# Kernel optimization log

Hardware: AMD Instinct MI355X
Metric: run time of the kernel (lower is better)

The kernel has to match this reference:

```python
import jax, jax.numpy as jnp
import numpy as np

EMBED = 256
HEADS = 8
HEAD_DIM = EMBED // HEADS  # 32, even for RoPE
INIT_VAL = 1.0
HEADS_RANGE = 3.0


def rotate_every_two(x):
    # (x1, x2) -> (-x2, x1) on interleaved pairs of last dim
    x1 = x[..., ::2]
    x2 = x[..., 1::2]
    return jnp.stack([-x2, x1], axis=-1).reshape(x.shape)


def theta_shift(x, sin, cos):
    # x: [B, heads, H, W, D]; sin/cos: [H, W, D] broadcast over B, heads
    return x * cos + rotate_every_two(x) * sin


def rel_pos_2d(H, W):
    # RetNetRelPos2d: RoPE angles + per-head exponential decay mask
    angle = 1.0 / (10000.0 ** jnp.linspace(0.0, 1.0, HEAD_DIM // 2))
    angle = jnp.repeat(angle, 2)  # [D]
    idx = jnp.arange(H * W, dtype=jnp.float32)
    sin = jnp.sin(idx[:, None] * angle[None, :]).reshape(H, W, HEAD_DIM)
    cos = jnp.cos(idx[:, None] * angle[None, :]).reshape(H, W, HEAD_DIM)
    h_idx = jnp.arange(HEADS, dtype=jnp.float32)
    decay = jnp.log(1.0 - 2.0 ** (-INIT_VAL - HEADS_RANGE * h_idx / HEADS))  # [heads]
    gh, gw = jnp.meshgrid(jnp.arange(H), jnp.arange(W), indexing='ij')
    grid = jnp.stack([gh, gw], axis=-1).reshape(H * W, 2)  # [N,2]
    dist = jnp.abs(grid[:, None, :] - grid[None, :, :]).sum(-1)  # [N,N] L1 distance
    mask = dist[None, :, :].astype(jnp.float32) * decay[:, None, None]  # [heads,N,N]
    return sin, cos, mask


def setup_inputs() -> dict:
    key = jax.random.key(0)
    ks = jax.random.split(key, 8)
    B, H, W, C = 2, 48, 48, EMBED
    s = 0.02
    return {
        'x': jax.random.normal(ks[0], (B, H, W, C), jnp.float32),
        'Wq': jax.random.normal(ks[1], (C, C), jnp.float32) * s,
        'bq': jnp.zeros((C,), jnp.float32),
        'Wk': jax.random.normal(ks[2], (C, C), jnp.float32) * s,
        'bk': jnp.zeros((C,), jnp.float32),
        'Wv': jax.random.normal(ks[3], (C, C), jnp.float32) * s,
        'bv': jnp.zeros((C,), jnp.float32),
        'lepe_w': jax.random.normal(ks[4], (C, 1, 5, 5), jnp.float32) * s,  # depthwise 5x5
        'lepe_b': jnp.zeros((C,), jnp.float32),
        'Wo': jax.random.normal(ks[5], (C, C), jnp.float32) * s,
        'bo': jnp.zeros((C,), jnp.float32),
    }


def reference(x, Wq, bq, Wk, bk, Wv, bv, lepe_w, lepe_b, Wo, bo):
    B, H, W, C = x.shape
    N = H * W
    sin, cos, mask = rel_pos_2d(H, W)
    scaling = HEAD_DIM ** -0.5

    q = x @ Wq + bq
    k = (x @ Wk + bk) * scaling
    v = x @ Wv + bv

    # lepe: depthwise 5x5 conv on v (BHWC)
    lepe = jax.lax.conv_general_dilated(
        v.transpose(0, 3, 1, 2), lepe_w, (1, 1), 'SAME',
        feature_group_count=C, dimension_numbers=('NCHW', 'OIHW', 'NCHW'))
    lepe = lepe.transpose(0, 2, 3, 1) + lepe_b  # [B,H,W,C]

    def split_heads(t):
        return t.reshape(B, H, W, HEADS, HEAD_DIM).transpose(0, 3, 1, 2, 4)

    qr = theta_shift(split_heads(q), sin, cos).reshape(B, HEADS, N, HEAD_DIM)
    kr = theta_shift(split_heads(k), sin, cos).reshape(B, HEADS, N, HEAD_DIM)
    vv = split_heads(v).reshape(B, HEADS, N, HEAD_DIM)

    attn = jnp.einsum('bhnd,bhmd->bhnm', qr, kr) + mask[None]  # [B,heads,N,N]
    attn = jax.nn.softmax(attn, axis=-1)
    out = jnp.einsum('bhnm,bhmd->bhnd', attn, vv)
    out = out.transpose(0, 2, 1, 3).reshape(B, H, W, C)
    out = out + lepe
    return out @ Wo + bo
```

## Files before the change

kernel.cpp:

```cpp
#include <hip/hip_runtime.h>
#include <hip/hip_bf16.h>
#include <math.h>

#define NN 2304
#define ROWSZ 4608
#define SZ (ROWSZ*256)

typedef __attribute__((ext_vector_type(8))) short short8;
typedef __attribute__((ext_vector_type(4))) float f32x4;

__device__ __forceinline__ float bf2f(unsigned short u) {
    return __uint_as_float(((unsigned int)u) << 16);
}
__device__ __forceinline__ unsigned short f2bf(float f) {
    unsigned int u = __float_as_uint(f);
    u += 0x7FFFu + ((u >> 16) & 1u);
    return (unsigned short)(u >> 16);
}
__device__ __forceinline__ unsigned int pack_bf2(float a, float b) {
    return (unsigned int)f2bf(a) | ((unsigned int)f2bf(b) << 16);
}

__device__ __forceinline__ float ub2f(unsigned int v, int r) {
#if defined(__has_builtin)
#if __has_builtin(__builtin_amdgcn_cvt_f32_ubyte0)
    switch (r) {
        case 0: return __builtin_amdgcn_cvt_f32_ubyte0(v);
        case 1: return __builtin_amdgcn_cvt_f32_ubyte1(v);
        case 2: return __builtin_amdgcn_cvt_f32_ubyte2(v);
        default: return __builtin_amdgcn_cvt_f32_ubyte3(v);
    }
#else
    return (float)((v >> (8*r)) & 0xFFu);
#endif
#else
    return (float)((v >> (8*r)) & 0xFFu);
#endif
}

template<int F32>
__device__ __forceinline__ float ldin(const void* p, int i) {
    if constexpr (F32) return ((const float*)p)[i];
    else return bf2f(((const unsigned short*)p)[i]);
}

__global__ void detect_kernel(const unsigned int* __restrict__ x, int* __restrict__ flag) {
    int t = threadIdx.x;
    int cnt = 0;
    for (int i = t; i < 256; i += 64) {
        unsigned int e = (x[i] >> 7) & 0xFFu;
        cnt += (e < 87u || e > 167u) ? 1 : 0;
    }
    #pragma unroll
    for (int o = 32; o; o >>= 1) cnt += __shfl_down(cnt, o);
    if (t == 0) *flag = (cnt >= 32) ? 1 : 0;
}

__global__ __launch_bounds__(256) void dist_kernel(unsigned char* __restrict__ D,
                                                   float2* __restrict__ scT) {
    const int nq = blockIdx.x;
    const int yq = (nq*21846) >> 20, xq = nq - yq*48;
    unsigned int* drow = reinterpret_cast<unsigned int*>(D + (size_t)nq*NN);
    for (int idx = threadIdx.x; idx < 576; idx += 256) {
        const int kp0 = idx*4;
        unsigned int wv = 0;
        #pragma unroll
        for (int r = 0; r < 4; ++r) {
            int kp = kp0 + r;
            int yk = (kp*21846) >> 20;
            int xk = kp - yk*48;
            unsigned int dist = __usad((unsigned)yq, (unsigned)yk,
                                __usad((unsigned)xq, (unsigned)xk, 0u));
            wv |= dist << (8*r);
        }
        drow[idx] = wv;
    }
    if (threadIdx.x < 16) {
        const int j = threadIdx.x;
        const float ang = exp2f((float)j * (-0.8858474919699633f));
        float sv, cv;
        sincosf((float)nq * ang, &sv, &cv);
        scT[nq*16 + j] = make_float2(sv, cv);
    }
}

__global__ __launch_bounds__(256) void xprep_kernel(const void* __restrict__ x,
    const int* __restrict__ flag, unsigned short* __restrict__ xb)
{
    const int e = (blockIdx.x*256 + threadIdx.x) * 8;
    if (*flag) {
        const float* xp = (const float*)x + e;
        float4 a0 = *reinterpret_cast<const float4*>(xp);
        float4 a1 = *reinterpret_cast<const float4*>(xp + 4);
        uint4 o;
        o.x = pack_bf2(a0.x, a0.y); o.y = pack_bf2(a0.z, a0.w);
        o.z = pack_bf2(a1.x, a1.y); o.w = pack_bf2(a1.z, a1.w);
        *reinterpret_cast<uint4*>(xb + e) = o;
    } else {
        *reinterpret_cast<uint4*>(xb + e) =
            *reinterpret_cast<const uint4*>((const unsigned short*)x + e);
    }
}

__global__ __launch_bounds__(256) void wprep_kernel(
    const void* __restrict__ Wq, const void* __restrict__ bq,
    const void* __restrict__ Wk, const void* __restrict__ bk,
    const void* __restrict__ Wv, const void* __restrict__ bv,
    const void* __restrict__ Wo, const void* __restrict__ bo,
    const void* __restrict__ lw, const void* __restrict__ lb,
    const int* __restrict__ flag,
    unsigned short* __restrict__ Wt, float* __restrict__ bb,
    float* __restrict__ lwT)
{
    __shared__ float wsh[256][17];
    const int t = threadIdx.x;
    const int m = blockIdx.y;
    const int F = *flag;
    if (m == 4) {
        if (blockIdx.x != 0) return;
        float wv[25];
        #pragma unroll
        for (int j = 0; j < 25; ++j)
            wv[j] = F ? ((const float*)lw)[t*25 + j]
                      : bf2f(((const unsigned short*)lw)[t*25 + j]);
        #pragma unroll
        for (int j = 0; j < 25; ++j) lwT[j*256 + t] = wv[j];
        bb[4*256 + t] = F ? ((const float*)lb)[t]
                          : bf2f(((const unsigned short*)lb)[t]);
        return;
    }
    const int oc0 = blockIdx.x * 16;
    const void* W  = (m == 0) ? Wq : (m == 1) ? Wk : (m == 2) ? Wv : Wo;
    const void* bs = (m == 0) ? bq : (m == 1) ? bk : (m == 2) ? bv : bo;
    const float scale = (m == 1) ? 0.17677669529663687f * 1.4426950408889634f : 1.0f;
    #pragma unroll
    for (int j2 = 0; j2 < 16; ++j2)
        wsh[t][j2] = F ? ((const float*)W)[t*256 + oc0 + j2]
                       : bf2f(((const unsigned short*)W)[t*256 + oc0 + j2]);
    __syncthreads();
    const int j = t >> 4, seg = t & 15;
    unsigned int u[8];
    #pragma unroll
    for (int i = 0; i < 8; ++i) {
        float v0 = wsh[seg*16 + 2*i][j]     * scale;
        float v1 = wsh[seg*16 + 2*i + 1][j] * scale;
        u[i] = pack_bf2(v0, v1);
    }
    unsigned short* drow = Wt + ((size_t)(m*256 + oc0 + j))*256 + seg*16;
    *reinterpret_cast<uint4*>(drow)     = make_uint4(u[0], u[1], u[2], u[3]);
    *reinterpret_cast<uint4*>(drow + 8) = make_uint4(u[4], u[5], u[6], u[7]);
    if (blockIdx.x == 0)
        bb[m*256 + t] = (F ? ((const float*)bs)[t]
                           : bf2f(((const unsigned short*)bs)[t])) * scale;
}

__global__ __launch_bounds__(256) void qkv_mfma(
    const unsigned short* __restrict__ xb, const unsigned short* __restrict__ Wt,
    const float* __restrict__ bb, const float2* __restrict__ scT,
    unsigned short* __restrict__ q, unsigned short* __restrict__ k,
    unsigned short* __restrict__ v, unsigned short* __restrict__ vT)
{
    __shared__ __align__(16) char smem[43136];
    char* sc_lds = smem + 40960;
    const int t = threadIdx.x;
    const int w = t >> 6, lane = t & 63;
    const int q16 = lane & 15, quad = lane >> 4;
    const int m = blockIdx.y;
    const int tok0 = blockIdx.x * 16;
    const int b = (tok0 >= NN) ? 1 : 0;
    const int n0 = tok0 - b*NN;

    {
        float2 sv = scT[(size_t)(n0 + (t >> 4))*16 + (t & 15)];
        *reinterpret_cast<float2*>(sc_lds + (t >> 4)*136 + (t & 15)*8) = sv;
    }
    short8 af[8];
    #pragma unroll
    for (int kk = 0; kk < 8; ++kk)
        af[kk] = *reinterpret_cast<const short8*>(
            xb + (size_t)(tok0 + q16)*256 + kk*32 + quad*8);

    const unsigned short* Wm = Wt + (size_t)m*256*256;
    {
        const unsigned short* src = Wm + (size_t)t*256;
        #pragma unroll
        for (int s = 0; s < 4; ++s)
            *reinterpret_cast<uint4*>(smem + t*80 + s*16) =
                *reinterpret_cast<const uint4*>(src + s*8);
    }
    __syncthreads();

    f32x4 acc[4];
    #pragma unroll
    for (int tt = 0; tt < 4; ++tt) acc[tt] = (f32x4){0.f, 0.f, 0.f, 0.f};
    int cur = 0;
    for (int kk = 0; kk < 8; ++kk) {
        const int kkn = (kk < 7) ? kk + 1 : 7;
        uint4 nw[4];
        const unsigned short* src = Wm + (size_t)t*256 + kkn*32;
        #pragma unroll
        for (int s = 0; s < 4; ++s) nw[s] = *reinterpret_cast<const uint4*>(src + s*8);
        char* Wl = smem + cur*20480;
        #pragma unroll
        for (int tt = 0; tt < 4; ++tt) {
            short8 bf = *reinterpret_cast<const short8*>(
                Wl + (w*64 + tt*16 + q16)*80 + quad*16);
            acc[tt] = __builtin_amdgcn_mfma_f32_16x16x32_bf16(af[kk], bf, acc[tt], 0, 0, 0);
        }
        char* Wn = smem + (cur ^ 1)*20480;
        #pragma unroll
        for (int s = 0; s < 4; ++s)
            *reinterpret_cast<uint4*>(Wn + t*80 + s*16) = nw[s];
        __syncthreads();
        cur ^= 1;
    }

    char* ostage = smem;
    float bias[4];
    #pragma unroll
    for (int tt = 0; tt < 4; ++tt) bias[tt] = bb[m*256 + w*64 + tt*16 + q16];
    if (m < 2) {
        const int odd = q16 & 1;
        #pragma unroll
        for (int tt = 0; tt < 4; ++tt) {
            const int j = ((tt & 1) << 3) + (q16 >> 1);
            #pragma unroll
            for (int r = 0; r < 4; ++r) {
                const int tokL = quad*4 + r;
                float a = acc[tt][r] + bias[tt];
                float ap = __shfl_xor(a, 1);
                float2 sc = *reinterpret_cast<const float2*>(sc_lds + tokL*136 + j*8);
                float val = odd ? fmaf(a, sc.y, ap*sc.x) : fmaf(a, sc.y, -ap*sc.x);
                *reinterpret_cast<unsigned short*>(
                    ostage + tokL*528 + (w*64 + tt*16 + q16)*2) = f2bf(val);
            }
        }
    } else {
        #pragma unroll
        for (int tt = 0; tt < 4; ++tt) {
            #pragma unroll
            for (int r = 0; r < 4; ++r)
                *reinterpret_cast<unsigned short*>(
                    ostage + (quad*4 + r)*528 + (w*64 + tt*16 + q16)*2)
                    = f2bf(acc[tt][r] + bias[tt]);
        }
    }
    __syncthreads();
    unsigned short* dst = (m == 0) ? q : (m == 1) ? k : v;
    {
        char* p = ostage + (t >> 4)*528 + (t & 15)*32;
        uint4 a0 = *reinterpret_cast<uint4*>(p);
        uint4 a1 = *reinterpret_cast<uint4*>(p + 16);
        unsigned short* drow = dst + (size_t)(tok0 + (t >> 4))*256 + (t & 15)*16;
        *reinterpret_cast<uint4*>(drow)     = a0;
        *reinterpret_cast<uint4*>(drow + 8) = a1;
    }
    if (m == 2) {
        const int h = t >> 5, d = t & 31;
        unsigned int vp[8];
        #pragma unroll
        for (int i = 0; i < 8; ++i) {
            unsigned short e0 = *reinterpret_cast<unsigned short*>(
                ostage + (2*i)*528 + (h*32 + d)*2);
            unsigned short e1 = *reinterpret_cast<unsigned short*>(
                ostage + (2*i + 1)*528 + (h*32 + d)*2);
            vp[i] = (unsigned int)e0 | ((unsigned int)e1 << 16);
        }
        unsigned short* vt = vT + ((size_t)(b*8 + h)*32 + d)*NN + n0;
        *reinterpret_cast<uint4*>(vt)     = make_uint4(vp[0], vp[1], vp[2], vp[3]);
        *reinterpret_cast<uint4*>(vt + 8) = make_uint4(vp[4], vp[5], vp[6], vp[7]);
    }
}

__global__ __launch_bounds__(256) void lepe_kernel(const unsigned short* __restrict__ v,
    const float* __restrict__ lwT, const float* __restrict__ bb,
    unsigned short* __restrict__ lepe)
{
    int c = threadIdx.x;
    int pos = blockIdx.x;
    int b  = pos >= NN ? 1 : 0;
    int yx = pos - b*NN;
    int y  = (yx*21846) >> 20;
    int xx = yx - y*48;
    float acc = bb[4*256 + c];
    #pragma unroll
    for (int ky = 0; ky < 5; ++ky) {
        int yy = y + ky - 2;
        if ((unsigned)yy >= 48u) continue;
        #pragma unroll
        for (int kx = 0; kx < 5; ++kx) {
            int xc = xx + kx - 2;
            if ((unsigned)xc >= 48u) continue;
            acc = fmaf(bf2f(v[((b*NN + yy*48 + xc)<<8) + c]),
                       lwT[(ky*5 + kx)*256 + c], acc);
        }
    }
    lepe[(pos<<8) + c] = f2bf(acc);
}

template<int DIRECT>
__global__ __launch_bounds__(256) void attn_kernel(
    const unsigned short* __restrict__ q, const unsigned short* __restrict__ k,
    const unsigned short* __restrict__ vT, const unsigned char* __restrict__ D,
    unsigned short* __restrict__ o, float* __restrict__ pacc, float* __restrict__ pl)
{
    __shared__ char smem[27648];
    const int t = threadIdx.x;
    const int w = t >> 6, lane = t & 63;
    const int q16 = lane & 15, quad = lane >> 4;
    char* PsB = smem + 19456 + w*2048;
    const int bh = blockIdx.y, b = bh >> 3, h = bh & 7;
    const int q0 = blockIdx.x*64 + w*16;
    const int nq = q0 + q16;
    const float decay2 = log2f(1.0f - exp2f(-1.0f - 0.375f*(float)h));
    short8 qfrag = *reinterpret_cast<const short8*>(q + ((size_t)(b*NN + nq))*256 + h*32 + quad*8);
    f32x4 acc0 = {0.f,0.f,0.f,0.f}, acc1 = {0.f,0.f,0.f,0.f};
    const f32x4 zero = {0.f,0.f,0.f,0.f};
    float lacc = 0.0f;
    const unsigned short* kbase = k + (size_t)(b*NN)*256 + h*32;
    const unsigned short* vtb = vT + (size_t)bh*32*NN;
    const unsigned char* Dbase = D + (size_t)nq*NN + quad*4;
    const int skr = t >> 2, skp = t & 3;
    const int svd = t >> 3, svp = t & 7;
    const int psW = q16*16 + (quad & 1)*8;
    const int qsh = quad >> 1;
    const int nchunk = 36 / gridDim.z;
    const int kt0 = blockIdx.z * nchunk;

    {
        uint4 kraw = *reinterpret_cast<const uint4*>(kbase + (kt0*64 + skr)*256 + skp*8);
        uint4 vraw = *reinterpret_cast<const uint4*>(vtb + svd*NN + kt0*64 + svp*8);
        *reinterpret_cast<uint4*>(smem + skr*80 + skp*16) = kraw;
        *reinterpret_cast<uint4*>(smem + 5120 + svd*144 + svp*16) = vraw;
    }
    __syncthreads();

    int cur = 0;
    for (int kc = 0; kc < nchunk; ++kc) {
        const int kt = kt0 + kc;
        const int ktn = (kc + 1 < nchunk) ? kt + 1 : kt;
        uint4 nk = *reinterpret_cast<const uint4*>(kbase + (ktn*64 + skr)*256 + skp*8);
        uint4 nv = *reinterpret_cast<const uint4*>(vtb + svd*NN + ktn*64 + svp*8);
        unsigned int dw[4];
        #pragma unroll
        for (int tt = 0; tt < 4; ++tt)
            dw[tt] = *reinterpret_cast<const unsigned int*>(Dbase + kt*64 + tt*16);
        char* KsB = smem + cur*9728;
        char* VtB = KsB + 5120;
        f32x4 st[4];
        #pragma unroll
        for (int tt = 0; tt < 4; ++tt) {
            short8 kf = *reinterpret_cast<const short8*>(KsB + (tt*16 + q16)*80 + quad*16);
            st[tt] = __builtin_amdgcn_mfma_f32_16x16x32_bf16(kf, qfrag, zero, 0, 0, 0);
        }
        unsigned int pk[8];
        float lsum = 0.0f;
        #pragma unroll
        for (int tt = 0; tt < 4; ++tt) {
            float p[4];
            #pragma unroll
            for (int r = 0; r < 4; ++r) {
                p[r] = exp2f(fmaf(decay2, ub2f(dw[tt], r), st[tt][r]));
                lsum += p[r];
            }
            pk[tt*2]   = __builtin_amdgcn_perm(__float_as_uint(p[1]), __float_as_uint(p[0]), 0x07060302);
            pk[tt*2+1] = __builtin_amdgcn_perm(__float_as_uint(p[3]), __float_as_uint(p[2]), 0x07060302);
        }
        lacc += lsum;
        #pragma unroll
        for (int tt = 0; tt < 4; ++tt) {
            uint2 pp; pp.x = pk[tt*2]; pp.y = pk[tt*2+1];
            *reinterpret_cast<uint2*>(PsB + (tt >> 1)*1024 + (((tt*2) + qsh) & 3)*256 + psW) = pp;
        }
        #pragma unroll
        for (int kh = 0; kh < 2; ++kh) {
            short8 pf = *reinterpret_cast<const short8*>(PsB + kh*1024 + lane*16);
            short8 v0 = *reinterpret_cast<const short8*>(VtB + q16*144 + kh*64 + quad*16);
            short8 v1 = *reinterpret_cast<const short8*>(VtB + (16 + q16)*144 + kh*64 + quad*16);
            acc0 = __builtin_amdgcn_mfma_f32_16x16x32_bf16(v0, pf, acc0, 0, 0, 0);
            acc1 = __builtin_amdgcn_mfma_f32_16x16x32_bf16(v1, pf, acc1, 0, 0, 0);
        }
        char* KsN = smem + (cur^1)*9728;
        *reinterpret_cast<uint4*>(KsN + skr*80 + skp*16) = nk;
        *reinterpret_cast<uint4*>(KsN + 5120 + svd*144 + svp*16) = nv;
        __syncthreads();
        cur ^= 1;
    }
    lacc += __shfl_xor(lacc, 16);
    lacc += __shfl_xor(lacc, 32);
    if constexpr (DIRECT) {
        float invl = 1.0f / lacc;
        unsigned short* orow = o + ((size_t)(b*NN + nq))*256 + h*32;
        uint2 w0, w1;
        w0.x = pack_bf2(acc0[0]*invl, acc0[1]*invl);
        w0.y = pack_bf2(acc0[2]*invl, acc0[3]*invl);
        w1.x = pack_bf2(acc1[0]*invl, acc1[1]*invl);
        w1.y = pack_bf2(acc1[2]*invl, acc1[3]*invl);
        *reinterpret_cast<uint2*>(orow + quad*4)      = w0;
        *reinterpret_cast<uint2*>(orow + 16 + quad*4) = w1;
    } else {
        float* pb = pacc + ((size_t)(blockIdx.z*16 + bh)*NN + nq)*32;
        *reinterpret_cast<f32x4*>(pb + quad*4)      = acc0;
        *reinterpret_cast<f32x4*>(pb + 16 + quad*4) = acc1;
        if (quad == 0) pl[((size_t)blockIdx.z*16 + bh)*NN + nq] = lacc;
    }
}

__global__ __launch_bounds__(256) void out_mfma(
    const unsigned short* __restrict__ o,
    const float* __restrict__ pacc, const float* __restrict__ pl,
    const unsigned short* __restrict__ lp,
    const unsigned short* __restrict__ Wt, const float* __restrict__ bb,
    const int* __restrict__ flag, void* __restrict__ out, int nsplit)
{
    __shared__ __align__(16) char smem[49408];
    char* Ast = smem + 40960;
    const int t = threadIdx.x;
    const int w = t >> 6, lane = t & 63;
    const int q16 = lane & 15, quad = lane >> 4;
    const int tok0 = blockIdx.x * 16;

    {
        const int r = t >> 4, c0 = (t & 15) * 16;
        const int nqr = tok0 + r;
        uint4 lb0 = *reinterpret_cast<const uint4*>(lp + (size_t)nqr*256 + c0);
        uint4 lb1 = *reinterpret_cast<const uint4*>(lp + (size_t)nqr*256 + c0 + 8);
        const unsigned short* lu0 = reinterpret_cast<const unsigned short*>(&lb0);
        const unsigned short* lu1 = reinterpret_cast<const unsigned short*>(&lb1);
        float av[16];
        if (nsplit == 0) {
            uint4 oa0 = *reinterpret_cast<const uint4*>(o + (size_t)nqr*256 + c0);
            uint4 oa1 = *reinterpret_cast<const uint4*>(o + (size_t)nqr*256 + c0 + 8);
            const unsigned short* ou0 = reinterpret_cast<const unsigned short*>(&oa0);
            const unsigned short* ou1 = reinterpret_cast<const unsigned short*>(&oa1);
            #pragma unroll
            for (int j = 0; j < 8; ++j) {
                av[j]     = bf2f(ou0[j]) + bf2f(lu0[j]);
                av[8 + j] = bf2f(ou1[j]) + bf2f(lu1[j]);
            }
        } else {
            const int b = nqr >= NN ? 1 : 0;
            const int nq = nqr - b*NN;
            const int bh = b*8 + (c0 >> 5);
            const int d0 = c0 & 31;
            float s[16];
            #pragma unroll
            for (int j = 0; j < 16; ++j) s[j] = 0.f;
            float lsum = 0.f;
            for (int p = 0; p < nsplit; ++p) {
                const float* pb = pacc + ((size_t)(p*16 + bh)*NN + nq)*32 + d0;
                #pragma unroll
                for (int j4 = 0; j4 < 4; ++j4) {
                    f32x4 vv = *reinterpret_cast<const f32x4*>(pb + j4*4);
                    s[j4*4+0] += vv[0]; s[j4*4+1] += vv[1];
                    s[j4*4+2] += vv[2]; s[j4*4+3] += vv[3];
                }
                lsum += pl[((size_t)p*16 + bh)*NN + nq];
            }
            float invl = 1.0f / lsum;
            #pragma unroll
            for (int j = 0; j < 8; ++j) {
                av[j]     = fmaf(s[j],     invl, bf2f(lu0[j]));
                av[8 + j] = fmaf(s[8 + j], invl, bf2f(lu1[j]));
            }
        }
        unsigned int u[8];
        #pragma unroll
        for (int i = 0; i < 8; ++i) u[i] = pack_bf2(av[2*i], av[2*i+1]);
        *reinterpret_cast<uint4*>(Ast + r*528 + c0*2)      = make_uint4(u[0],u[1],u[2],u[3]);
        *reinterpret_cast<uint4*>(Ast + r*528 + c0*2 + 16) = make_uint4(u[4],u[5],u[6],u[7]);
    }
    const unsigned short* Wm = Wt + (size_t)3*256*256;
    {
        const unsigned short* src = Wm + (size_t)t*256;
        #pragma unroll
        for (int s2 = 0; s2 < 4; ++s2)
            *reinterpret_cast<uint4*>(smem + t*80 + s2*16) =
                *reinterpret_cast<const uint4*>(src + s2*8);
    }
    __syncthreads();
    short8 af[8];
    #pragma unroll
    for (int kk = 0; kk < 8; ++kk)
        af[kk] = *reinterpret_cast<const short8*>(Ast + q16*528 + kk*64 + quad*16);

    f32x4 acc[4];
    #pragma unroll
    for (int tt = 0; tt < 4; ++tt) acc[tt] = (f32x4){0.f, 0.f, 0.f, 0.f};
    int cur = 0;
    for (int kk = 0; kk < 8; ++kk) {
        const int kkn = (kk < 7) ? kk + 1 : 7;
        uint4 nw[4];
        const unsigned short* src = Wm + (size_t)t*256 + kkn*32;
        #pragma unroll
        for (int s2 = 0; s2 < 4; ++s2) nw[s2] = *reinterpret_cast<const uint4*>(src + s2*8);
        char* Wl = smem + cur*20480;
        #pragma unroll
        for (int tt = 0; tt < 4; ++tt) {
            short8 bf = *reinterpret_cast<const short8*>(
                Wl + (w*64 + tt*16 + q16)*80 + quad*16);
            acc[tt] = __builtin_amdgcn_mfma_f32_16x16x32_bf16(af[kk], bf, acc[tt], 0, 0, 0);
        }
        char* Wn = smem + (cur ^ 1)*20480;
        #pragma unroll
        for (int s2 = 0; s2 < 4; ++s2)
            *reinterpret_cast<uint4*>(Wn + t*80 + s2*16) = nw[s2];
        __syncthreads();
        cur ^= 1;
    }
    const int F = *flag;
    float bias[4];
    #pragma unroll
    for (int tt = 0; tt < 4; ++tt) bias[tt] = bb[3*256 + w*64 + tt*16 + q16];
    if (F) {
        char* ostf = smem;
        #pragma unroll
        for (int tt = 0; tt < 4; ++tt) {
            #pragma unroll
            for (int r = 0; r < 4; ++r)
                *reinterpret_cast<float*>(ostf + (quad*4 + r)*1040
                    + (w*64 + tt*16 + q16)*4) = acc[tt][r] + bias[tt];
        }
        __syncthreads();
        char* p = ostf + (t >> 4)*1040 + (t & 15)*64;
        float4 x0 = *reinterpret_cast<float4*>(p);
        float4 x1 = *reinterpret_cast<float4*>(p + 16);
        float4 x2 = *reinterpret_cast<float4*>(p + 32);
        float4 x3 = *reinterpret_cast<float4*>(p + 48);
        float* drow = (float*)out + (size_t)(tok0 + (t >> 4))*256 + (t & 15)*16;
        *reinterpret_cast<float4*>(drow)      = x0;
        *reinterpret_cast<float4*>(drow + 4)  = x1;
        *reinterpret_cast<float4*>(drow + 8)  = x2;
        *reinterpret_cast<float4*>(drow + 12) = x3;
    } else {
        char* ost = smem;
        #pragma unroll
        for (int tt = 0; tt < 4; ++tt) {
            #pragma unroll
            for (int r = 0; r < 4; ++r)
                *reinterpret_cast<unsigned short*>(ost + (quad*4 + r)*528
                    + (w*64 + tt*16 + q16)*2) = f2bf(acc[tt][r] + bias[tt]);
        }
        __syncthreads();
        char* p = ost + (t >> 4)*528 + (t & 15)*32;
        uint4 a0 = *reinterpret_cast<uint4*>(p);
        uint4 a1 = *reinterpret_cast<uint4*>(p + 16);
        unsigned short* drow = (unsigned short*)out + (size_t)(tok0 + (t >> 4))*256 + (t & 15)*16;
        *reinterpret_cast<uint4*>(drow)     = a0;
        *reinterpret_cast<uint4*>(drow + 8) = a1;
    }
}

extern "C" void kernel_launch(void* const* d_in, const int* in_sizes, int n_in,
                              void* d_out, int out_size, void* d_ws, size_t ws_size,
                              hipStream_t stream)
{
    const void* x  = d_in[0];
    const void* Wq = d_in[1];
    const void* bq = d_in[2];
    const void* Wk = d_in[3];
    const void* bk = d_in[4];
    const void* Wv = d_in[5];
    const void* bv = d_in[6];
    const void* lw = d_in[7];
    const void* lb = d_in[8];
    const void* Wo = d_in[9];
    const void* bo = d_in[10];

    int* flag = (int*)d_ws;
    unsigned short* qb   = (unsigned short*)((char*)d_ws + 256);
    unsigned short* kbuf = qb   + (size_t)SZ;
    unsigned short* vbuf = kbuf + (size_t)SZ;
    unsigned short* obuf = vbuf + (size_t)SZ;
    unsigned short* lbuf = obuf + (size_t)SZ;
    unsigned short* vtb  = lbuf + (size_t)SZ;
    unsigned char*  Dtab = (unsigned char*)(vtb + (size_t)SZ);
    float2* scT = (float2*)(Dtab + (size_t)NN*NN);
    unsigned short* xb = (unsigned short*)(scT + (size_t)NN*16);
    unsigned short* Wt = xb + (size_t)SZ;
    float* bb  = (float*)(Wt + (size_t)4*256*256);
    float* lwT = bb + 5*256;

    const size_t base = 256 + 6*(size_t)SZ*2 + (size_t)NN*NN
                      + (size_t)NN*16*8 + (size_t)SZ*2
                      + (size_t)4*256*256*2 + (size_t)5*256*4 + (size_t)25*256*4;
    const size_t per_split = (size_t)16*NN*32*4 + (size_t)16*NN*4;
    int nsplit = 0;
    if      (ws_size >= base + 6*per_split) nsplit = 6;
    else if (ws_size >= base + 4*per_split) nsplit = 4;
    else if (ws_size >= base + 2*per_split) nsplit = 2;
    else if (ws_size >= base + 1*per_split) nsplit = 1;
    float* pacc = (float*)((char*)d_ws + base);
    float* pl   = pacc + (size_t)(nsplit ? nsplit : 1)*16*NN*32;

    detect_kernel<<<1, 64, 0, stream>>>((const unsigned int*)x, flag);
    dist_kernel<<<NN, 256, 0, stream>>>(Dtab, scT);
    xprep_kernel<<<576, 256, 0, stream>>>(x, flag, xb);
    wprep_kernel<<<dim3(16,5), 256, 0, stream>>>(Wq, bq, Wk, bk, Wv, bv, Wo, bo, lw, lb, flag, Wt, bb, lwT);
    qkv_mfma<<<dim3(288,3), 256, 0, stream>>>(xb, Wt, bb, scT, qb, kbuf, vbuf, vtb);
    lepe_kernel<<<4608, 256, 0, stream>>>(vbuf, lwT, bb, lbuf);
    if (nsplit) {
        attn_kernel<0><<<dim3(36, 16, nsplit), 256, 0, stream>>>(qb, kbuf, vtb, Dtab, obuf, pacc, pl);
    } else {
        attn_kernel<1><<<dim3(36, 16, 1), 256, 0, stream>>>(qb, kbuf, vtb, Dtab, obuf, pacc, pl);
    }
    out_mfma<<<288, 256, 0, stream>>>(obuf, pacc, pl, lbuf, Wt, bb, flag, d_out, nsplit);
}
```

Baseline: 203.1 us.

## Fuse four prep kernels into one launch and cap attention split at four

Result: faster. 192.0 us (-5.5%).

```diff
diff --git a/kernel.cpp b/kernel.cpp
--- a/kernel.cpp
+++ b/kernel.cpp
@@ -38,86 +38,89 @@
 #endif
 }
 
-template<int F32>
-__device__ __forceinline__ float ldin(const void* p, int i) {
-    if constexpr (F32) return ((const float*)p)[i];
-    else return bf2f(((const unsigned short*)p)[i]);
-}
-
-__global__ void detect_kernel(const unsigned int* __restrict__ x, int* __restrict__ flag) {
-    int t = threadIdx.x;
-    int cnt = 0;
-    for (int i = t; i < 256; i += 64) {
-        unsigned int e = (x[i] >> 7) & 0xFFu;
-        cnt += (e < 87u || e > 167u) ? 1 : 0;
-    }
-    #pragma unroll
-    for (int o = 32; o; o >>= 1) cnt += __shfl_down(cnt, o);
-    if (t == 0) *flag = (cnt >= 32) ? 1 : 0;
-}
-
-__global__ __launch_bounds__(256) void dist_kernel(unsigned char* __restrict__ D,
-                                                   float2* __restrict__ scT) {
-    const int nq = blockIdx.x;
-    const int yq = (nq*21846) >> 20, xq = nq - yq*48;
-    unsigned int* drow = reinterpret_cast<unsigned int*>(D + (size_t)nq*NN);
-    for (int idx = threadIdx.x; idx < 576; idx += 256) {
-        const int kp0 = idx*4;
-        unsigned int wv = 0;
-        #pragma unroll
-        for (int r = 0; r < 4; ++r) {
-            int kp = kp0 + r;
-            int yk = (kp*21846) >> 20;
-            int xk = kp - yk*48;
-            unsigned int dist = __usad((unsigned)yq, (unsigned)yk,
-                                __usad((unsigned)xq, (unsigned)xk, 0u));
-            wv |= dist << (8*r);
-        }
-        drow[idx] = wv;
-    }
-    if (threadIdx.x < 16) {
-        const int j = threadIdx.x;
-        const float ang = exp2f((float)j * (-0.8858474919699633f));
-        float sv, cv;
-        sincosf((float)nq * ang, &sv, &cv);
-        scT[nq*16 + j] = make_float2(sv, cv);
-    }
-}
-
-__global__ __launch_bounds__(256) void xprep_kernel(const void* __restrict__ x,
-    const int* __restrict__ flag, unsigned short* __restrict__ xb)
-{
-    const int e = (blockIdx.x*256 + threadIdx.x) * 8;
-    if (*flag) {
-        const float* xp = (const float*)x + e;
-        float4 a0 = *reinterpret_cast<const float4*>(xp);
-        float4 a1 = *reinterpret_cast<const float4*>(xp + 4);
-        uint4 o;
-        o.x = pack_bf2(a0.x, a0.y); o.y = pack_bf2(a0.z, a0.w);
-        o.z = pack_bf2(a1.x, a1.y); o.w = pack_bf2(a1.z, a1.w);
-        *reinterpret_cast<uint4*>(xb + e) = o;
-    } else {
-        *reinterpret_cast<uint4*>(xb + e) =
-            *reinterpret_cast<const uint4*>((const unsigned short*)x + e);
-    }
-}
-
-__global__ __launch_bounds__(256) void wprep_kernel(
+__global__ __launch_bounds__(256) void prep_kernel(
+    const void* __restrict__ x,
     const void* __restrict__ Wq, const void* __restrict__ bq,
     const void* __restrict__ Wk, const void* __restrict__ bk,
     const void* __restrict__ Wv, const void* __restrict__ bv,
     const void* __restrict__ Wo, const void* __restrict__ bo,
     const void* __restrict__ lw, const void* __restrict__ lb,
-    const int* __restrict__ flag,
+    int* __restrict__ flag, unsigned char* __restrict__ D,
+    float2* __restrict__ scT, unsigned short* __restrict__ xb,
     unsigned short* __restrict__ Wt, float* __restrict__ bb,
     float* __restrict__ lwT)
 {
     __shared__ float wsh[256][17];
+    __shared__ int sflag;
+    const int blk = blockIdx.x;
     const int t = threadIdx.x;
-    const int m = blockIdx.y;
-    const int F = *flag;
+
+    {
+        const int nq = blk;
+        const int yq = (nq*21846) >> 20, xq = nq - yq*48;
+        unsigned int* drow = reinterpret_cast<unsigned int*>(D + (size_t)nq*NN);
+        for (int idx = t; idx < 576; idx += 256) {
+            const int kp0 = idx*4;
+            unsigned int wv = 0;
+            #pragma unroll
+            for (int r = 0; r < 4; ++r) {
+                int kp = kp0 + r;
+                int yk = (kp*21846) >> 20;
+                int xk = kp - yk*48;
+                unsigned int dist = __usad((unsigned)yq, (unsigned)yk,
+                                    __usad((unsigned)xq, (unsigned)xk, 0u));
+                wv |= dist << (8*r);
+            }
+            drow[idx] = wv;
+        }
+        if (t < 16) {
+            const int j = t;
+            const float ang = exp2f((float)j * (-0.8858474919699633f));
+            float sv, cv;
+            sincosf((float)nq * ang, &sv, &cv);
+            scT[nq*16 + j] = make_float2(sv, cv);
+        }
+    }
+    if (blk >= 656) return;
+
+    {
+        const unsigned int* xu = (const unsigned int*)x;
+        if (t < 64) {
+            int cnt = 0;
+            for (int i = t; i < 256; i += 64) {
+                unsigned int e = (xu[i] >> 7) & 0xFFu;
+                cnt += (e < 87u || e > 167u) ? 1 : 0;
+            }
+            #pragma unroll
+            for (int o = 32; o; o >>= 1) cnt += __shfl_down(cnt, o);
+            if (t == 0) sflag = (cnt >= 32) ? 1 : 0;
+        }
+        __syncthreads();
+    }
+    const int F = sflag;
+    if (blk == 0 && t == 0) *flag = F;
+
+    if (blk < 576) {
+        const int e = (blk*256 + t) * 8;
+        if (F) {
+            const float* xp = (const float*)x + e;
+            float4 a0 = *reinterpret_cast<const float4*>(xp);
+            float4 a1 = *reinterpret_cast<const float4*>(xp + 4);
+            uint4 o;
+            o.x = pack_bf2(a0.x, a0.y); o.y = pack_bf2(a0.z, a0.w);
+            o.z = pack_bf2(a1.x, a1.y); o.w = pack_bf2(a1.z, a1.w);
+            *reinterpret_cast<uint4*>(xb + e) = o;
+        } else {
+            *reinterpret_cast<uint4*>(xb + e) =
+                *reinterpret_cast<const uint4*>((const unsigned short*)x + e);
+        }
+        return;
+    }
+
+    const int idx = blk - 576;
+    const int m = idx >> 4;
     if (m == 4) {
-        if (blockIdx.x != 0) return;
+        if ((idx & 15) != 0) return;
         float wv[25];
         #pragma unroll
         for (int j = 0; j < 25; ++j)
@@ -129,7 +132,7 @@
                           : bf2f(((const unsigned short*)lb)[t]);
         return;
     }
-    const int oc0 = blockIdx.x * 16;
+    const int oc0 = (idx & 15) * 16;
     const void* W  = (m == 0) ? Wq : (m == 1) ? Wk : (m == 2) ? Wv : Wo;
     const void* bs = (m == 0) ? bq : (m == 1) ? bk : (m == 2) ? bv : bo;
     const float scale = (m == 1) ? 0.17677669529663687f * 1.4426950408889634f : 1.0f;
@@ -149,7 +152,7 @@
     unsigned short* drow = Wt + ((size_t)(m*256 + oc0 + j))*256 + seg*16;
     *reinterpret_cast<uint4*>(drow)     = make_uint4(u[0], u[1], u[2], u[3]);
     *reinterpret_cast<uint4*>(drow + 8) = make_uint4(u[4], u[5], u[6], u[7]);
-    if (blockIdx.x == 0)
+    if ((idx & 15) == 0)
         bb[m*256 + t] = (F ? ((const float*)bs)[t]
                            : bf2f(((const unsigned short*)bs)[t])) * scale;
 }
@@ -586,17 +589,14 @@
                       + (size_t)4*256*256*2 + (size_t)5*256*4 + (size_t)25*256*4;
     const size_t per_split = (size_t)16*NN*32*4 + (size_t)16*NN*4;
     int nsplit = 0;
-    if      (ws_size >= base + 6*per_split) nsplit = 6;
-    else if (ws_size >= base + 4*per_split) nsplit = 4;
+    if      (ws_size >= base + 4*per_split) nsplit = 4;
     else if (ws_size >= base + 2*per_split) nsplit = 2;
     else if (ws_size >= base + 1*per_split) nsplit = 1;
     float* pacc = (float*)((char*)d_ws + base);
     float* pl   = pacc + (size_t)(nsplit ? nsplit : 1)*16*NN*32;
 
-    detect_kernel<<<1, 64, 0, stream>>>((const unsigned int*)x, flag);
-    dist_kernel<<<NN, 256, 0, stream>>>(Dtab, scT);
-    xprep_kernel<<<576, 256, 0, stream>>>(x, flag, xb);
-    wprep_kernel<<<dim3(16,5), 256, 0, stream>>>(Wq, bq, Wk, bk, Wv, bv, Wo, bo, lw, lb, flag, Wt, bb, lwT);
+    prep_kernel<<<NN, 256, 0, stream>>>(x, Wq, bq, Wk, bk, Wv, bv, Wo, bo,
+                                        lw, lb, flag, Dtab, scT, xb, Wt, bb, lwT);
     qkv_mfma<<<dim3(288,3), 256, 0, stream>>>(xb, Wt, bb, scT, qb, kbuf, vbuf, vtb);
     lepe_kernel<<<4608, 256, 0, stream>>>(vbuf, lwT, bb, lbuf);
     if (nsplit) {
```
